# Performance work log

Hardware: AMD Instinct MI355X
Metric: run time of the kernel (lower is better)

Reference implementation:

```python
import jax, jax.numpy as jnp
import numpy as np

N_RAYS = 8192
M = 524288
GX, GY, GZ = 160, 160, 128
NFEAT = 12
POS_PE, VIEW_PE = 10, 4
WIDTH = 128
POS_DIM = 3 + 3 * POS_PE * 2      # 63
VIEW_DIM = 3 + 3 * VIEW_PE * 2    # 27
DIM0 = NFEAT + POS_DIM            # 75
ACT_SHIFT = float(np.log(1.0 / (1.0 - 1e-6) - 1.0))  # density bias shift from alpha_init
INTERVAL = 0.5                    # stepsize * voxel_size_ratio
XYZ_MIN, XYZ_MAX = -1.0, 1.0


def posemb(x, n_pe):
    # x: [N,3] -> [N, 3 + 3*n_pe*2], matching cat([x, sin(x*freq), cos(x*freq)])
    freq = 2.0 ** jnp.arange(n_pe, dtype=x.dtype)
    xf = (x[..., None] * freq).reshape(x.shape[0], -1)
    return jnp.concatenate([x, jnp.sin(xf), jnp.cos(xf)], axis=-1)


def trilinear(grid, xyz):
    # grid: [X,Y,Z,C]; xyz: [M,3] in world coords. align_corners=True bilinear (grid_sample).
    sz_f = jnp.array(grid.shape[:3], jnp.float32)
    sz_i = jnp.array(grid.shape[:3], jnp.int32)
    t = (xyz - XYZ_MIN) / (XYZ_MAX - XYZ_MIN) * (sz_f - 1.0)
    t = jnp.clip(t, 0.0, sz_f - 1.0)
    i0 = jnp.clip(jnp.floor(t).astype(jnp.int32), 0, sz_i - 2)
    f = t - i0.astype(t.dtype)
    out = jnp.zeros((xyz.shape[0], grid.shape[-1]), t.dtype)
    for dx in (0, 1):
        for dy in (0, 1):
            for dz in (0, 1):
                w = ((f[:, 0] if dx else 1.0 - f[:, 0])
                     * (f[:, 1] if dy else 1.0 - f[:, 1])
                     * (f[:, 2] if dz else 1.0 - f[:, 2]))
                out = out + w[:, None] * grid[i0[:, 0] + dx, i0[:, 1] + dy, i0[:, 2] + dz]
    return out


def mask_lookup(mask, xyz):
    # nearest-neighbor maskcache_lookup: ijk = round(xyz*scale + shift)
    sz_f = jnp.array(mask.shape, jnp.float32)
    scale = (sz_f - 1.0) / (XYZ_MAX - XYZ_MIN)
    shift = -XYZ_MIN * scale
    ijk = jnp.clip(jnp.round(xyz * scale + shift).astype(jnp.int32), 0,
                   jnp.array(mask.shape, jnp.int32) - 1)
    return mask[ijk[:, 0], ijk[:, 1], ijk[:, 2]]


def alphas2weights(alpha, ray_id, n_rays):
    # segmented T_i = prod_{j<i in ray}(1-alpha_j); weights = T*alpha (ray_id sorted)
    log1a = jnp.log(jnp.clip(1.0 - alpha, 1e-10, 1.0))
    excl = jnp.cumsum(log1a) - log1a                      # global exclusive cumsum
    seg_tot = jax.ops.segment_sum(log1a, ray_id, num_segments=n_rays)
    seg_start = jnp.cumsum(seg_tot) - seg_tot             # exclusive prefix over rays
    T = jnp.exp(excl - seg_start[ray_id])
    weights = T * alpha
    alphainv_last = jnp.exp(seg_tot)
    return weights, alphainv_last


def setup_inputs() -> dict:
    key = jax.random.key(0)
    ks = jax.random.split(key, 16)
    xyz = jax.random.uniform(ks[0], (M, 3), jnp.float32) * (XYZ_MAX - XYZ_MIN) + XYZ_MIN
    ray_id = jnp.sort(jax.random.randint(ks[1], (M,), 0, N_RAYS))
    viewdirs = jax.random.normal(ks[2], (N_RAYS, 3), jnp.float32)
    viewdirs = viewdirs / jnp.linalg.norm(viewdirs, axis=-1, keepdims=True)
    mask = jax.random.uniform(ks[3], (GX, GY, GZ)) > 0.1
    density = jax.random.normal(ks[4], (GX, GY, GZ), jnp.float32) * 0.5
    k0 = jax.random.normal(ks[5], (GX, GY, GZ, NFEAT), jnp.float32) * 0.1
    s = 0.05
    W0 = jax.random.normal(ks[6], (DIM0, WIDTH), jnp.float32) * s
    b0 = jnp.zeros((WIDTH,), jnp.float32)
    W1 = jax.random.normal(ks[7], (WIDTH, WIDTH), jnp.float32) * s
    b1 = jnp.zeros((WIDTH,), jnp.float32)
    W2 = jax.random.normal(ks[8], (WIDTH, WIDTH), jnp.float32) * s
    b2 = jnp.zeros((WIDTH,), jnp.float32)
    Wr = jax.random.normal(ks[9], (WIDTH + VIEW_DIM, 3), jnp.float32) * s
    br = jnp.zeros((3,), jnp.float32)
    return {"xyz": xyz, "ray_id": ray_id, "viewdirs": viewdirs, "mask": mask,
            "density": density, "k0": k0, "W0": W0, "b0": b0, "W1": W1, "b1": b1,
            "W2": W2, "b2": b2, "Wr": Wr, "br": br}


def reference(xyz, ray_id, viewdirs, mask, density, k0, W0, b0, W1, b1, W2, b2, Wr, br):
    # 1) empty-space skipping via mask cache (kept as multiplicative mask for static shapes)
    m = mask_lookup(mask, xyz).astype(xyz.dtype)
    # 2) trilinear density query + raw2alpha
    d = trilinear(density[..., None], xyz)[:, 0]
    alpha = 1.0 - (1.0 + jnp.exp(d + ACT_SHIFT)) ** (-INTERVAL)
    alpha = alpha * m
    # 3) segmented alpha compositing (Alphas2Weights)
    weights, alphainv_last = alphas2weights(alpha, ray_id, N_RAYS)
    # 4) feature query + view MLP -> rgb
    feat = trilinear(k0, xyz)                              # [M, NFEAT]
    h = jnp.concatenate([feat, posemb(xyz, POS_PE)], -1)   # [M, DIM0]
    h = jax.nn.relu(h @ W0 + b0)
    h = jax.nn.relu(h @ W1 + b1)
    h = jax.nn.relu(h @ W2 + b2)
    ve = posemb(viewdirs, VIEW_PE)[ray_id]                 # [M, VIEW_DIM]
    rgb = jax.nn.sigmoid(jnp.concatenate([h, ve], -1) @ Wr + br)
    # 5) composite per ray + white background
    rgb_marched = jax.ops.segment_sum(weights[:, None] * rgb, ray_id, num_segments=N_RAYS)
    rgb_marched = rgb_marched + alphainv_last[:, None] * 1.0
    return rgb_marched
```

## Files before the change

### kernel.cpp

```cpp
#include <hip/hip_runtime.h>
#include <hip/hip_bf16.h>

#define M_SAMPLES 524288
#define NRAYS 8192
#define GXD 160
#define GYD 160
#define GZD 128
#define GYZ (GYD*GZD)
#define NVOX (GXD*GYD*GZD)
#define ACT_SHIFT -13.81550955796f
#define ROWA 136
#define ROWB 136
#define SAMP 64

typedef __bf16 bf16x8 __attribute__((ext_vector_type(8)));
typedef float f32x4 __attribute__((ext_vector_type(4)));
typedef float f32x16 __attribute__((ext_vector_type(16)));
typedef float f32v2 __attribute__((ext_vector_type(2)));

static __device__ inline unsigned short f2bf(float f){
  __hip_bfloat16 h = __float2bfloat16(f);
  unsigned short u; __builtin_memcpy(&u, &h, 2); return u;
}
static __device__ inline float flo(unsigned int u){ return __uint_as_float(u << 16); }
static __device__ inline float fhi(unsigned int u){ return __uint_as_float(u & 0xffff0000u); }

#if defined(__has_builtin)
#if __has_builtin(__builtin_amdgcn_cvt_pk_bf16_f32)
#define HAVE_PK_BF16 1
#endif
#if __has_builtin(__builtin_amdgcn_cvt_pk_f32_fp8) && __has_builtin(__builtin_amdgcn_cvt_pk_fp8_f32)
#define HAVE_FP8 1
#endif
#endif

static __device__ inline unsigned int packbf(float a, float b){
#ifdef HAVE_PK_BF16
  typedef __bf16 bf16v2 __attribute__((ext_vector_type(2)));
  bf16v2 r = __builtin_amdgcn_cvt_pk_bf16_f32(a, b);
  unsigned int u; __builtin_memcpy(&u, &r, 4); return u;
#else
  return (unsigned int)f2bf(a) | ((unsigned int)f2bf(b) << 16);
#endif
}

struct Tri {
  int ix, iy, iz;
  float wx0, wx1, wy0, wy1, wz0, wz1;
};
static __device__ inline Tri tri_setup(float x, float y, float z){
  Tri t;
  float tx = (x+1.f)*0.5f*(float)(GXD-1); tx = fminf(fmaxf(tx,0.f),(float)(GXD-1));
  float ty = (y+1.f)*0.5f*(float)(GYD-1); ty = fminf(fmaxf(ty,0.f),(float)(GYD-1));
  float tz = (z+1.f)*0.5f*(float)(GZD-1); tz = fminf(fmaxf(tz,0.f),(float)(GZD-1));
  t.ix = min((int)tx, GXD-2); t.iy = min((int)ty, GYD-2); t.iz = min((int)tz, GZD-2);
  float fx = tx-t.ix, fy = ty-t.iy, fz = tz-t.iz;
  t.wx0 = 1.f-fx; t.wx1 = fx; t.wy0 = 1.f-fy; t.wy1 = fy; t.wz0 = 1.f-fz; t.wz1 = fz;
  return t;
}

#define NB_REPACK (NVOX/256)
#define NB_W      184
#define NB_RT     (NRAYS/256)
__global__ __launch_bounds__(256) void k_prep(
    const float* __restrict__ density, const float* __restrict__ k0,
    uint4* __restrict__ packed,
    const unsigned int* __restrict__ mw, int* __restrict__ flag,
    const float* __restrict__ W0, const float* __restrict__ W1,
    const float* __restrict__ W2, const float* __restrict__ Wr,
    const float* __restrict__ br,
    unsigned short* __restrict__ wt0, unsigned short* __restrict__ wt1,
    unsigned short* __restrict__ wt2, unsigned short* __restrict__ wtr,
    const float* __restrict__ vd, float* __restrict__ rayterm3)
{
  int b = blockIdx.x;
  if(b < NB_REPACK){
    int v = b*256 + threadIdx.x;
    const float4* kp = (const float4*)(k0 + (size_t)v*12);
    float4 a = kp[0], bb = kp[1], c = kp[2];
#ifdef HAVE_FP8
    uint4 o;
    o.x = __float_as_uint(density[v]);
    int w;
    w = __builtin_amdgcn_cvt_pk_fp8_f32(a.x, a.y, 0, false);
    w = __builtin_amdgcn_cvt_pk_fp8_f32(a.z, a.w, w, true);
    o.y = (unsigned int)w;
    w = __builtin_amdgcn_cvt_pk_fp8_f32(bb.x, bb.y, 0, false);
    w = __builtin_amdgcn_cvt_pk_fp8_f32(bb.z, bb.w, w, true);
    o.z = (unsigned int)w;
    w = __builtin_amdgcn_cvt_pk_fp8_f32(c.x, c.y, 0, false);
    w = __builtin_amdgcn_cvt_pk_fp8_f32(c.z, c.w, w, true);
    o.w = (unsigned int)w;
    packed[v] = o;
#else
    uint4 o0, o1;
    o0.x = __float_as_uint(density[v]);
    o0.y = packbf(a.x, a.y); o0.z = packbf(a.z, a.w); o0.w = packbf(bb.x, bb.y);
    o1.x = packbf(bb.z, bb.w); o1.y = packbf(c.x, c.y); o1.z = packbf(c.z, c.w);
    o1.w = 0;
    packed[(size_t)v*2]   = o0;
    packed[(size_t)v*2+1] = o1;
#endif
    return;
  }
  if(b == NB_REPACK){
    unsigned int v = mw[threadIdx.x & 63];
    unsigned long long any = __ballot(v > 1u);
    if(threadIdx.x == 0) *flag = (any != 0ull) ? 1 : 0;
    return;
  }
  if(b < NB_REPACK + 1 + NB_W){
    int t = (b - NB_REPACK - 1)*256 + threadIdx.x;
    if(t < 128*96){
      int n = t/96, k = t%96;
      wt0[t] = f2bf((k < 75) ? W0[k*128 + n] : 0.f);
    } else if(t < 128*96 + 16384){
      int j = t - 128*96; int n = j/128, k = j%128;
      wt1[j] = f2bf(W1[k*128 + n]);
    } else if(t < 128*96 + 32768){
      int j = t - 128*96 - 16384; int n = j/128, k = j%128;
      wt2[j] = f2bf(W2[k*128 + n]);
    } else if(t < 128*96 + 32768 + 16*128){
      int j = t - 128*96 - 32768; int n = j/128, k = j%128;
      wtr[j] = f2bf((n < 3) ? Wr[k*3 + n] : 0.f);
    }
    return;
  }
  int ray = (b - NB_REPACK - 1 - NB_W)*256 + threadIdx.x;
  if(ray >= NRAYS) return;
  float v0 = vd[ray*3+0], v1 = vd[ray*3+1], v2 = vd[ray*3+2];
  float vej[27];
  vej[0] = v0; vej[1] = v1; vej[2] = v2;
  #pragma unroll
  for(int ci = 0; ci < 3; ++ci){
    float xv = (ci == 0) ? v0 : ((ci == 1) ? v1 : v2);
    #pragma unroll
    for(int p = 0; p < 4; ++p){
      float arg = xv * (float)(1 << p);
      vej[3 + ci*4 + p]  = __sinf(arg);
      vej[15 + ci*4 + p] = __cosf(arg);
    }
  }
  float rt0 = br[0], rt1 = br[1], rt2 = br[2];
  #pragma unroll
  for(int j = 0; j < 27; ++j){
    const float* wr = Wr + (128 + j)*3;
    rt0 += vej[j]*wr[0]; rt1 += vej[j]*wr[1]; rt2 += vej[j]*wr[2];
  }
  rayterm3[ray*3+0] = rt0; rayterm3[ray*3+1] = rt1; rayterm3[ray*3+2] = rt2;
}

template<int KDIM, int SROW>
static __device__ __forceinline__ void mfma_layer(const unsigned short* src,
    const bf16x8* wf, f32x16& acc0, f32x16& acc1, int ln, int kh)
{
  constexpr int NS = KDIM/16;
  const unsigned short* abase0 = src + (ln)*SROW + kh*8;
  const unsigned short* abase1 = src + (32 + ln)*SROW + kh*8;
  f32x16 z = {0.f,0.f,0.f,0.f,0.f,0.f,0.f,0.f,0.f,0.f,0.f,0.f,0.f,0.f,0.f,0.f};
  acc0 = z; acc1 = z;
  __builtin_amdgcn_s_setprio(1);
  #pragma unroll
  for(int st = 0; st < NS; ++st){
    bf16x8 a0 = *(const bf16x8*)(abase0 + st*16);
    bf16x8 a1 = *(const bf16x8*)(abase1 + st*16);
    acc0 = __builtin_amdgcn_mfma_f32_32x32x16_bf16(wf[st], a0, acc0, 0, 0, 0);
    acc1 = __builtin_amdgcn_mfma_f32_32x32x16_bf16(wf[st], a1, acc1, 0, 0, 0);
  }
  __builtin_amdgcn_s_setprio(0);
}

template<int NS>
static __device__ __forceinline__ void load_wf(const unsigned short* wbase, bf16x8* wf){
  #pragma unroll
  for(int st = 0; st < NS; ++st) wf[st] = *(const bf16x8*)(wbase + st*16);
}

template<int DROW>
static __device__ __forceinline__ void epilogue(const f32x16& acc0, const f32x16& acc1,
    unsigned short* dst, const float* __restrict__ bias, int tile_n, int ln, int kh)
{
  float4 bv[4];
  #pragma unroll
  for(int g = 0; g < 4; ++g) bv[g] = *(const float4*)(bias + tile_n*32 + g*8 + kh*4);
  #pragma unroll
  for(int rep = 0; rep < 2; ++rep){
    const f32x16& acc = rep ? acc1 : acc0;
    int scol = rep*32 + ln;
    #pragma unroll
    for(int g = 0; g < 4; ++g){
      int n0 = tile_n*32 + g*8 + kh*4;
      unsigned int lo = packbf(fmaxf(acc[4*g+0] + bv[g].x, 0.f), fmaxf(acc[4*g+1] + bv[g].y, 0.f));
      unsigned int hi = packbf(fmaxf(acc[4*g+2] + bv[g].z, 0.f), fmaxf(acc[4*g+3] + bv[g].w, 0.f));
      unsigned long long o = (unsigned long long)lo | ((unsigned long long)hi << 32);
      *(unsigned long long*)(dst + scol*DROW + n0) = o;
    }
  }
}

template<int PACKED>
__global__ __launch_bounds__(256, 4) void k_mlp(const float* __restrict__ xyz,
    const uint4* __restrict__ packed,
    const float* __restrict__ density, const float* __restrict__ k0,
    const void* __restrict__ mask, const int* __restrict__ flag,
    const int* __restrict__ ray_id,
    const unsigned short* __restrict__ wt0, const unsigned short* __restrict__ wt1,
    const unsigned short* __restrict__ wt2, const unsigned short* __restrict__ wtr,
    const float* __restrict__ b0, const float* __restrict__ b1,
    const float* __restrict__ b2,
    const float* __restrict__ rayterm3, float4* __restrict__ rgba_out)
{
  __shared__ alignas(16) unsigned short hA[SAMP*ROWA];
  __shared__ alignas(16) unsigned short hB[SAMP*ROWB];
  __shared__ float red[SAMP][4];
  __shared__ int ray_s[SAMP];

  int tid = threadIdx.x;
  int lane = tid & 63, wave = tid >> 6;
  int blk = blockIdx.x*SAMP;
  int ln = lane & 31, kh = lane >> 5;

  bf16x8 wf[8];
  load_wf<6>(wt0 + (wave*32 + ln)*96 + kh*8, wf);

  {
    int smp = tid >> 2, corner = tid & 3;
    int i = blk + smp;
    float x = xyz[3*i+0], y = xyz[3*i+1], z = xyz[3*i+2];
    Tri t = tri_setup(x, y, z);
    int dx = corner & 1, dy = corner >> 1;
    float wxy = (dx ? t.wx1 : t.wx0) * (dy ? t.wy1 : t.wy0);
    float w0 = wxy*t.wz0, w1 = wxy*t.wz1;
    size_t vox = (size_t)((t.ix+dx)*GYZ + (t.iy+dy)*GZD + t.iz);
    float pd;
    float pf[12];
#ifdef HAVE_FP8
    if(PACKED){
      uint4 q0 = packed[vox], q1 = packed[vox+1];
      pd = w0*__uint_as_float(q0.x) + w1*__uint_as_float(q1.x);
      f32v2 a, b;
      a = __builtin_amdgcn_cvt_pk_f32_fp8((int)q0.y, false);
      b = __builtin_amdgcn_cvt_pk_f32_fp8((int)q1.y, false);
      pf[0] = w0*a.x + w1*b.x;  pf[1] = w0*a.y + w1*b.y;
      a = __builtin_amdgcn_cvt_pk_f32_fp8((int)q0.y, true);
      b = __builtin_amdgcn_cvt_pk_f32_fp8((int)q1.y, true);
      pf[2] = w0*a.x + w1*b.x;  pf[3] = w0*a.y + w1*b.y;
      a = __builtin_amdgcn_cvt_pk_f32_fp8((int)q0.z, false);
      b = __builtin_amdgcn_cvt_pk_f32_fp8((int)q1.z, false);
      pf[4] = w0*a.x + w1*b.x;  pf[5] = w0*a.y + w1*b.y;
      a = __builtin_amdgcn_cvt_pk_f32_fp8((int)q0.z, true);
      b = __builtin_amdgcn_cvt_pk_f32_fp8((int)q1.z, true);
      pf[6] = w0*a.x + w1*b.x;  pf[7] = w0*a.y + w1*b.y;
      a = __builtin_amdgcn_cvt_pk_f32_fp8((int)q0.w, false);
      b = __builtin_amdgcn_cvt_pk_f32_fp8((int)q1.w, false);
      pf[8] = w0*a.x + w1*b.x;  pf[9] = w0*a.y + w1*b.y;
      a = __builtin_amdgcn_cvt_pk_f32_fp8((int)q0.w, true);
      b = __builtin_amdgcn_cvt_pk_f32_fp8((int)q1.w, true);
      pf[10]= w0*a.x + w1*b.x;  pf[11]= w0*a.y + w1*b.y;
    }
#else
    if(PACKED){
      const uint4* pv = packed + vox*2;
      uint4 q0 = pv[0], q1 = pv[1], q2 = pv[2], q3 = pv[3];
      pd = w0*__uint_as_float(q0.x) + w1*__uint_as_float(q2.x);
      pf[0]  = w0*flo(q0.y) + w1*flo(q2.y);  pf[1]  = w0*fhi(q0.y) + w1*fhi(q2.y);
      pf[2]  = w0*flo(q0.z) + w1*flo(q2.z);  pf[3]  = w0*fhi(q0.z) + w1*fhi(q2.z);
      pf[4]  = w0*flo(q0.w) + w1*flo(q2.w);  pf[5]  = w0*fhi(q0.w) + w1*fhi(q2.w);
      pf[6]  = w0*flo(q1.x) + w1*flo(q3.x);  pf[7]  = w0*fhi(q1.x) + w1*fhi(q3.x);
      pf[8]  = w0*flo(q1.y) + w1*flo(q3.y);  pf[9]  = w0*fhi(q1.y) + w1*fhi(q3.y);
      pf[10] = w0*flo(q1.z) + w1*flo(q3.z);  pf[11] = w0*fhi(q1.z) + w1*fhi(q3.z);
    }
#endif
    if(!PACKED){
      pd = w0*density[vox] + w1*density[vox+1];
      const float4* v = (const float4*)(k0 + vox*12);
      float4 a0 = v[0], a1 = v[1], a2 = v[2];
      float4 c0 = v[3], c1 = v[4], c2 = v[5];
      pf[0] = w0*a0.x + w1*c0.x;  pf[1] = w0*a0.y + w1*c0.y;
      pf[2] = w0*a0.z + w1*c0.z;  pf[3] = w0*a0.w + w1*c0.w;
      pf[4] = w0*a1.x + w1*c1.x;  pf[5] = w0*a1.y + w1*c1.y;
      pf[6] = w0*a1.z + w1*c1.z;  pf[7] = w0*a1.w + w1*c1.w;
      pf[8] = w0*a2.x + w1*c2.x;  pf[9] = w0*a2.y + w1*c2.y;
      pf[10]= w0*a2.z + w1*c2.z;  pf[11]= w0*a2.w + w1*c2.w;
    }
    #pragma unroll
    for(int m2 = 1; m2 < 4; m2 <<= 1){
      pd += __shfl_xor(pd, m2);
      #pragma unroll
      for(int j = 0; j < 12; ++j) pf[j] += __shfl_xor(pf[j], m2);
    }
    if(corner == 0){
      int mx = (int)rintf(x*79.5f + 79.5f); mx = min(max(mx,0), GXD-1);
      int my = (int)rintf(y*79.5f + 79.5f); my = min(max(my,0), GYD-1);
      int mz = (int)rintf(z*63.5f + 63.5f); mz = min(max(mz,0), GZD-1);
      int midx = mx*GYZ + my*GZD + mz;
      bool mm = (*flag) ? (((const unsigned char*)mask)[midx] != 0)
                        : (((const int*)mask)[midx] != 0);
      float e = __expf(pd + ACT_SHIFT);
      float alpha = 1.f - rsqrtf(1.f + e);
      if(!mm) alpha = 0.f;
      red[smp][3] = alpha;
      unsigned int d[8];
      #pragma unroll
      for(int j = 0; j < 6; ++j) d[j] = packbf(pf[2*j], pf[2*j+1]);
      d[6] = packbf(x, y);
      d[7] = packbf(z, __sinf(x));
      uint4* p = (uint4*)(hA + smp*ROWA);
      p[0] = make_uint4(d[0],d[1],d[2],d[3]);
      p[1] = make_uint4(d[4],d[5],d[6],d[7]);
    } else if(corner == 1){
      uint4* p = (uint4*)(hA + smp*ROWA + 80);
      p[0] = make_uint4(0,0,0,0);
      p[1] = make_uint4(0,0,0,0);
      ray_s[smp] = ray_id[i];
    }
  }

  {
    int smp = tid & 63, chunk = 1 + (tid >> 6);
    int i2 = blk + smp;
    float x = xyz[3*i2+0], y = xyz[3*i2+1], z = xyz[3*i2+2];
    float vv[16];
    #pragma unroll
    for(int j = 0; j < 16; ++j){
      int c = chunk*16 + j;
      float r;
      if(c >= 75) r = 0.f;
      else {
        int q = (c < 45) ? (c-15) : (c-45);
        int ci = q/10, p = q - ci*10;
        float xv = (ci == 0) ? x : ((ci == 1) ? y : z);
        float a = xv * (float)(1 << p);
        r = (c < 45) ? __sinf(a) : __cosf(a);
      }
      vv[j] = r;
    }
    unsigned int d[8];
    #pragma unroll
    for(int j = 0; j < 8; ++j) d[j] = packbf(vv[2*j], vv[2*j+1]);
    uint4* p = (uint4*)(hA + smp*ROWA + chunk*16);
    p[0] = make_uint4(d[0],d[1],d[2],d[3]);
    p[1] = make_uint4(d[4],d[5],d[6],d[7]);
  }
  __syncthreads();

  f32x16 acc0, acc1;

  mfma_layer<96, ROWA>(hA, wf, acc0, acc1, ln, kh);
  load_wf<8>(wt1 + (wave*32 + ln)*128 + kh*8, wf);
  epilogue<ROWB>(acc0, acc1, hB, b0, wave, ln, kh);
  __syncthreads();

  mfma_layer<128, ROWB>(hB, wf, acc0, acc1, ln, kh);
  load_wf<8>(wt2 + (wave*32 + ln)*128 + kh*8, wf);
  epilogue<ROWA>(acc0, acc1, hA, b1, wave, ln, kh);
  __syncthreads();

  int col = lane & 15, q4 = lane >> 4;
  mfma_layer<128, ROWA>(hA, wf, acc0, acc1, ln, kh);
  bf16x8 hw[4];
  {
    const unsigned short* wr = wtr + col*128 + q4*8;
    #pragma unroll
    for(int ks = 0; ks < 4; ++ks) hw[ks] = *(const bf16x8*)(wr + ks*32);
  }
  epilogue<ROWB>(acc0, acc1, hB, b2, wave, ln, kh);
  __syncthreads();

  {
    int mt = wave;
    f32x4 acc = {0.f, 0.f, 0.f, 0.f};
    const unsigned short* arow = hB + (mt*16 + col)*ROWB + q4*8;
    __builtin_amdgcn_s_setprio(1);
    #pragma unroll
    for(int ks = 0; ks < 4; ++ks){
      bf16x8 af = *(const bf16x8*)(arow + ks*32);
      acc = __builtin_amdgcn_mfma_f32_16x16x32_bf16(af, hw[ks], acc, 0, 0, 0);
    }
    __builtin_amdgcn_s_setprio(0);
    if(col < 3){
      #pragma unroll
      for(int r = 0; r < 4; ++r){
        int sl = mt*16 + q4*4 + r;
        float v = acc[r] + rayterm3[ray_s[sl]*3 + col];
        red[sl][col] = __fdividef(1.f, 1.f + __expf(-v));
      }
    }
  }
  __syncthreads();

  if(tid < SAMP){
    rgba_out[blk + tid] = make_float4(red[tid][0], red[tid][1], red[tid][2], red[tid][3]);
  }
}

__global__ __launch_bounds__(256) void k_comp2(const int* __restrict__ ray_id,
    const float4* __restrict__ rgba, float* __restrict__ out)
{
  int r = blockIdx.x*4 + (threadIdx.x >> 6);
  int lane = threadIdx.x & 63;
  int lo = 0, hi = M_SAMPLES;
  while(lo < hi){ int mid = (lo+hi) >> 1; if(ray_id[mid] < r) lo = mid+1; else hi = mid; }
  int s = lo;
  int lo2 = s, hi2 = M_SAMPLES;
  while(lo2 < hi2){ int mid = (lo2+hi2) >> 1; if(ray_id[mid] < r+1) lo2 = mid+1; else hi2 = mid; }
  int e = lo2;

  float carry = 1.f;
  float ar = 0.f, ag = 0.f, ab = 0.f;
  for(int base = s; base < e; base += 64){
    int idx = base + lane;
    float4 c = (idx < e) ? rgba[idx] : make_float4(0.f,0.f,0.f,0.f);
    float a = c.w;
    float incl = 1.f - a;
    #pragma unroll
    for(int d2 = 1; d2 < 64; d2 <<= 1){
      float t = __shfl_up(incl, d2);
      if(lane >= d2) incl *= t;
    }
    float excl = __shfl_up(incl, 1);
    if(lane == 0) excl = 1.f;
    float w = carry * excl * a;
    ar += w*c.x; ag += w*c.y; ab += w*c.z;
    carry *= __shfl(incl, 63);
  }
  #pragma unroll
  for(int m2 = 1; m2 < 64; m2 <<= 1){
    ar += __shfl_xor(ar, m2);
    ag += __shfl_xor(ag, m2);
    ab += __shfl_xor(ab, m2);
  }
  if(lane == 0){
    out[3*r+0] = ar + carry;
    out[3*r+1] = ag + carry;
    out[3*r+2] = ab + carry;
  }
}

extern "C" void kernel_launch(void* const* d_in, const int* in_sizes, int n_in,
                              void* d_out, int out_size, void* d_ws, size_t ws_size,
                              hipStream_t stream)
{
  const float* xyz      = (const float*)d_in[0];
  const int*   ray_id   = (const int*)  d_in[1];
  const float* viewdirs = (const float*)d_in[2];
  const void*  mask     =               d_in[3];
  const float* density  = (const float*)d_in[4];
  const float* k0       = (const float*)d_in[5];
  const float* W0 = (const float*)d_in[6];  const float* b0 = (const float*)d_in[7];
  const float* W1 = (const float*)d_in[8];  const float* b1 = (const float*)d_in[9];
  const float* W2 = (const float*)d_in[10]; const float* b2 = (const float*)d_in[11];
  const float* Wr = (const float*)d_in[12]; const float* br = (const float*)d_in[13];
  float* out = (float*)d_out;

  char* ws = (char*)d_ws;
  size_t off = 0;
  auto take = [&](size_t nbytes) -> void* {
    void* p = ws + off;
    off = (off + nbytes + 255) & ~(size_t)255;
    return p;
  };
  int*            flag     = (int*)           take(4);
  unsigned short* wt0      = (unsigned short*)take(128*96*2);
  unsigned short* wt1      = (unsigned short*)take(128*128*2);
  unsigned short* wt2      = (unsigned short*)take(128*128*2);
  unsigned short* wtr      = (unsigned short*)take(16*128*2);
  float*          rayterm3 = (float*)         take((size_t)NRAYS*3*4);
  float4*         rgba_ws  = (float4*)        take((size_t)M_SAMPLES*16);
#ifdef HAVE_FP8
  uint4*          packed   = (uint4*)         take((size_t)NVOX*16);
#else
  uint4*          packed   = (uint4*)         take((size_t)NVOX*32);
#endif
  bool use_packed = (ws_size >= off);

  k_prep<<<NB_REPACK + 1 + NB_W + NB_RT, 256, 0, stream>>>(
      density, k0, packed, (const unsigned int*)mask, flag,
      W0, W1, W2, Wr, br, wt0, wt1, wt2, wtr, viewdirs, rayterm3);
  if(use_packed){
    k_mlp<1><<<M_SAMPLES/SAMP, 256, 0, stream>>>(xyz, packed, density, k0, mask, flag,
                                                 ray_id, wt0, wt1, wt2, wtr,
                                                 b0, b1, b2, rayterm3, rgba_ws);
  } else {
    k_mlp<0><<<M_SAMPLES/SAMP, 256, 0, stream>>>(xyz, packed, density, k0, mask, flag,
                                                 ray_id, wt0, wt1, wt2, wtr,
                                                 b0, b1, b2, rayterm3, rgba_ws);
  }
  k_comp2<<<NRAYS/4, 256, 0, stream>>>(ray_id, rgba_ws, out);
}
```

Baseline: 417.1 us.

## Make MLP kernel persistent with register-resident weights and prefetched next-tile gathers

Converts k_mlp into a persistent kernel with 768 blocks that loop over the 64-sample tiles. Layer-1 and layer-2 weight fragments stay in registers across tiles, and biases are staged once in shared memory. Each iteration issues the next tile's xyz loads, grid gathers, mask lookup and ray_id load before running the current tile's MFMA layers, so gather latency overlaps compute. In exchange it uses many more registers, lowers occupancy to 3 blocks per SIMD group, and adds an extra barrier per tile.

```diff
diff --git a/kernel.cpp b/kernel.cpp
--- a/kernel.cpp
+++ b/kernel.cpp
@@ -12,6 +12,8 @@
 #define ROWA 136
 #define ROWB 136
 #define SAMP 64
+#define NTILES (M_SAMPLES/SAMP)
+#define GRID_MLP 768
 
 typedef __bf16 bf16x8 __attribute__((ext_vector_type(8)));
 typedef float f32x4 __attribute__((ext_vector_type(4)));
@@ -152,7 +154,7 @@
 
 template<int KDIM, int SROW>
 static __device__ __forceinline__ void mfma_layer(const unsigned short* src,
-    const bf16x8* wf, f32x16& acc0, f32x16& acc1, int ln, int kh)
+    const f32x4* wf, f32x16& acc0, f32x16& acc1, int ln, int kh)
 {
   constexpr int NS = KDIM/16;
   const unsigned short* abase0 = src + (ln)*SROW + kh*8;
@@ -164,25 +166,20 @@
   for(int st = 0; st < NS; ++st){
     bf16x8 a0 = *(const bf16x8*)(abase0 + st*16);
     bf16x8 a1 = *(const bf16x8*)(abase1 + st*16);
-    acc0 = __builtin_amdgcn_mfma_f32_32x32x16_bf16(wf[st], a0, acc0, 0, 0, 0);
-    acc1 = __builtin_amdgcn_mfma_f32_32x32x16_bf16(wf[st], a1, acc1, 0, 0, 0);
+    bf16x8 wv = __builtin_bit_cast(bf16x8, wf[st]);
+    acc0 = __builtin_amdgcn_mfma_f32_32x32x16_bf16(wv, a0, acc0, 0, 0, 0);
+    acc1 = __builtin_amdgcn_mfma_f32_32x32x16_bf16(wv, a1, acc1, 0, 0, 0);
   }
   __builtin_amdgcn_s_setprio(0);
-}
-
-template<int NS>
-static __device__ __forceinline__ void load_wf(const unsigned short* wbase, bf16x8* wf){
-  #pragma unroll
-  for(int st = 0; st < NS; ++st) wf[st] = *(const bf16x8*)(wbase + st*16);
 }
 
 template<int DROW>
 static __device__ __forceinline__ void epilogue(const f32x16& acc0, const f32x16& acc1,
-    unsigned short* dst, const float* __restrict__ bias, int tile_n, int ln, int kh)
+    unsigned short* dst, const float* sbias, int tile_n, int ln, int kh)
 {
   float4 bv[4];
   #pragma unroll
-  for(int g = 0; g < 4; ++g) bv[g] = *(const float4*)(bias + tile_n*32 + g*8 + kh*4);
+  for(int g = 0; g < 4; ++g) bv[g] = *(const float4*)(sbias + tile_n*32 + g*8 + kh*4);
   #pragma unroll
   for(int rep = 0; rep < 2; ++rep){
     const f32x16& acc = rep ? acc1 : acc0;
@@ -199,7 +196,7 @@
 }
 
 template<int PACKED>
-__global__ __launch_bounds__(256, 4) void k_mlp(const float* __restrict__ xyz,
+__global__ __launch_bounds__(256, 3) void k_mlp(const float* __restrict__ xyz,
     const uint4* __restrict__ packed,
     const float* __restrict__ density, const float* __restrict__ k0,
     const void* __restrict__ mask, const int* __restrict__ flag,
@@ -214,183 +211,257 @@
   __shared__ alignas(16) unsigned short hB[SAMP*ROWB];
   __shared__ float red[SAMP][4];
   __shared__ int ray_s[SAMP];
+  __shared__ alignas(16) float sb[384];
 
   int tid = threadIdx.x;
   int lane = tid & 63, wave = tid >> 6;
-  int blk = blockIdx.x*SAMP;
   int ln = lane & 31, kh = lane >> 5;
-
-  bf16x8 wf[8];
-  load_wf<6>(wt0 + (wave*32 + ln)*96 + kh*8, wf);
-
+  int col = lane & 15, q4 = lane >> 4;
+  int smp_a = tid >> 2, corner = tid & 3;
+  int dxc = corner & 1, dyc = corner >> 1;
+  int smp_b = tid & 63, chunk = 1 + (tid >> 6);
+  int flg = *flag;
+
+  if(tid < 96){
+    int which = tid >> 5, j = tid & 31;
+    const float* bs = (which == 0) ? b0 : ((which == 1) ? b1 : b2);
+    *(float4*)(sb + which*128 + j*4) = *(const float4*)(bs + j*4);
+  }
+
+  f32x4 wf1[8], wf2[8];
   {
-    int smp = tid >> 2, corner = tid & 3;
-    int i = blk + smp;
-    float x = xyz[3*i+0], y = xyz[3*i+1], z = xyz[3*i+2];
-    Tri t = tri_setup(x, y, z);
-    int dx = corner & 1, dy = corner >> 1;
-    float wxy = (dx ? t.wx1 : t.wx0) * (dy ? t.wy1 : t.wy0);
-    float w0 = wxy*t.wz0, w1 = wxy*t.wz1;
-    size_t vox = (size_t)((t.ix+dx)*GYZ + (t.iy+dy)*GZD + t.iz);
-    float pd;
-    float pf[12];
+    const unsigned short* w1b = wt1 + (wave*32 + ln)*128 + kh*8;
+    const unsigned short* w2b = wt2 + (wave*32 + ln)*128 + kh*8;
+    #pragma unroll
+    for(int st = 0; st < 8; ++st){
+      wf1[st] = *(const f32x4*)(w1b + st*16);
+      wf2[st] = *(const f32x4*)(w2b + st*16);
+    }
+  }
+  #pragma unroll
+  for(int st = 0; st < 8; ++st){
+    asm volatile("" : "+v"(wf1[st]));
+    asm volatile("" : "+v"(wf2[st]));
+  }
+
+  float ax, ay, az, bx, by, bz;
+  float cw0 = 0.f, cw1 = 0.f;
+  size_t voxs = 0;
+  uint4 q0 = {}, q1 = {};
+#ifndef HAVE_FP8
+  uint4 q2 = {}, q3 = {};
+#endif
+  int rid = 0; unsigned int mv = 0;
+
+  auto prefetch_gather = [&](int TT){
+    Tri tr = tri_setup(ax, ay, az);
+    float wxy = (dxc ? tr.wx1 : tr.wx0) * (dyc ? tr.wy1 : tr.wy0);
+    cw0 = wxy*tr.wz0; cw1 = wxy*tr.wz1;
+    voxs = (size_t)((tr.ix+dxc)*GYZ + (tr.iy+dyc)*GZD + tr.iz);
+    if(PACKED){
 #ifdef HAVE_FP8
-    if(PACKED){
-      uint4 q0 = packed[vox], q1 = packed[vox+1];
-      pd = w0*__uint_as_float(q0.x) + w1*__uint_as_float(q1.x);
-      f32v2 a, b;
-      a = __builtin_amdgcn_cvt_pk_f32_fp8((int)q0.y, false);
-      b = __builtin_amdgcn_cvt_pk_f32_fp8((int)q1.y, false);
-      pf[0] = w0*a.x + w1*b.x;  pf[1] = w0*a.y + w1*b.y;
-      a = __builtin_amdgcn_cvt_pk_f32_fp8((int)q0.y, true);
-      b = __builtin_amdgcn_cvt_pk_f32_fp8((int)q1.y, true);
-      pf[2] = w0*a.x + w1*b.x;  pf[3] = w0*a.y + w1*b.y;
-      a = __builtin_amdgcn_cvt_pk_f32_fp8((int)q0.z, false);
-      b = __builtin_amdgcn_cvt_pk_f32_fp8((int)q1.z, false);
-      pf[4] = w0*a.x + w1*b.x;  pf[5] = w0*a.y + w1*b.y;
-      a = __builtin_amdgcn_cvt_pk_f32_fp8((int)q0.z, true);
-      b = __builtin_amdgcn_cvt_pk_f32_fp8((int)q1.z, true);
-      pf[6] = w0*a.x + w1*b.x;  pf[7] = w0*a.y + w1*b.y;
-      a = __builtin_amdgcn_cvt_pk_f32_fp8((int)q0.w, false);
-      b = __builtin_amdgcn_cvt_pk_f32_fp8((int)q1.w, false);
-      pf[8] = w0*a.x + w1*b.x;  pf[9] = w0*a.y + w1*b.y;
-      a = __builtin_amdgcn_cvt_pk_f32_fp8((int)q0.w, true);
-      b = __builtin_amdgcn_cvt_pk_f32_fp8((int)q1.w, true);
-      pf[10]= w0*a.x + w1*b.x;  pf[11]= w0*a.y + w1*b.y;
-    }
+      q0 = packed[voxs]; q1 = packed[voxs+1];
 #else
-    if(PACKED){
-      const uint4* pv = packed + vox*2;
-      uint4 q0 = pv[0], q1 = pv[1], q2 = pv[2], q3 = pv[3];
-      pd = w0*__uint_as_float(q0.x) + w1*__uint_as_float(q2.x);
-      pf[0]  = w0*flo(q0.y) + w1*flo(q2.y);  pf[1]  = w0*fhi(q0.y) + w1*fhi(q2.y);
-      pf[2]  = w0*flo(q0.z) + w1*flo(q2.z);  pf[3]  = w0*fhi(q0.z) + w1*fhi(q2.z);
-      pf[4]  = w0*flo(q0.w) + w1*flo(q2.w);  pf[5]  = w0*fhi(q0.w) + w1*fhi(q2.w);
-      pf[6]  = w0*flo(q1.x) + w1*flo(q3.x);  pf[7]  = w0*fhi(q1.x) + w1*fhi(q3.x);
-      pf[8]  = w0*flo(q1.y) + w1*flo(q3.y);  pf[9]  = w0*fhi(q1.y) + w1*fhi(q3.y);
-      pf[10] = w0*flo(q1.z) + w1*flo(q3.z);  pf[11] = w0*fhi(q1.z) + w1*fhi(q3.z);
-    }
-#endif
-    if(!PACKED){
-      pd = w0*density[vox] + w1*density[vox+1];
-      const float4* v = (const float4*)(k0 + vox*12);
-      float4 a0 = v[0], a1 = v[1], a2 = v[2];
-      float4 c0 = v[3], c1 = v[4], c2 = v[5];
-      pf[0] = w0*a0.x + w1*c0.x;  pf[1] = w0*a0.y + w1*c0.y;
-      pf[2] = w0*a0.z + w1*c0.z;  pf[3] = w0*a0.w + w1*c0.w;
-      pf[4] = w0*a1.x + w1*c1.x;  pf[5] = w0*a1.y + w1*c1.y;
-      pf[6] = w0*a1.z + w1*c1.z;  pf[7] = w0*a1.w + w1*c1.w;
-      pf[8] = w0*a2.x + w1*c2.x;  pf[9] = w0*a2.y + w1*c2.y;
-      pf[10]= w0*a2.z + w1*c2.z;  pf[11]= w0*a2.w + w1*c2.w;
-    }
-    #pragma unroll
-    for(int m2 = 1; m2 < 4; m2 <<= 1){
-      pd += __shfl_xor(pd, m2);
-      #pragma unroll
-      for(int j = 0; j < 12; ++j) pf[j] += __shfl_xor(pf[j], m2);
+      const uint4* pv = packed + voxs*2;
+      q0 = pv[0]; q1 = pv[1]; q2 = pv[2]; q3 = pv[3];
+#endif
     }
     if(corner == 0){
-      int mx = (int)rintf(x*79.5f + 79.5f); mx = min(max(mx,0), GXD-1);
-      int my = (int)rintf(y*79.5f + 79.5f); my = min(max(my,0), GYD-1);
-      int mz = (int)rintf(z*63.5f + 63.5f); mz = min(max(mz,0), GZD-1);
+      int mx = (int)rintf(ax*79.5f + 79.5f); mx = min(max(mx,0), GXD-1);
+      int my = (int)rintf(ay*79.5f + 79.5f); my = min(max(my,0), GYD-1);
+      int mz = (int)rintf(az*63.5f + 63.5f); mz = min(max(mz,0), GZD-1);
       int midx = mx*GYZ + my*GZD + mz;
-      bool mm = (*flag) ? (((const unsigned char*)mask)[midx] != 0)
-                        : (((const int*)mask)[midx] != 0);
-      float e = __expf(pd + ACT_SHIFT);
-      float alpha = 1.f - rsqrtf(1.f + e);
-      if(!mm) alpha = 0.f;
-      red[smp][3] = alpha;
+      mv = flg ? (unsigned int)(((const unsigned char*)mask)[midx])
+               : ((const unsigned int*)mask)[midx];
+    } else if(corner == 1){
+      rid = ray_id[TT*SAMP + smp_a];
+    }
+  };
+
+  int t = blockIdx.x;
+  {
+    int ia = t*SAMP + smp_a;
+    ax = xyz[3*ia+0]; ay = xyz[3*ia+1]; az = xyz[3*ia+2];
+    int ib = t*SAMP + smp_b;
+    bx = xyz[3*ib+0]; by = xyz[3*ib+1]; bz = xyz[3*ib+2];
+  }
+  prefetch_gather(t);
+
+  for(; t < NTILES; t += GRID_MLP){
+    int nt = t + GRID_MLP;
+    bool has_next = nt < NTILES;
+    int blk = t*SAMP;
+
+    float nax=0.f, nay=0.f, naz=0.f, nbx=0.f, nby=0.f, nbz=0.f;
+    if(has_next){
+      int ia = nt*SAMP + smp_a;
+      nax = xyz[3*ia+0]; nay = xyz[3*ia+1]; naz = xyz[3*ia+2];
+      int ib = nt*SAMP + smp_b;
+      nbx = xyz[3*ib+0]; nby = xyz[3*ib+1]; nbz = xyz[3*ib+2];
+    }
+    __builtin_amdgcn_sched_barrier(0);
+
+    {
+      float pd;
+      float pf[12];
+#ifdef HAVE_FP8
+      if(PACKED){
+        pd = cw0*__uint_as_float(q0.x) + cw1*__uint_as_float(q1.x);
+        f32v2 a, b;
+        a = __builtin_amdgcn_cvt_pk_f32_fp8((int)q0.y, false);
+        b = __builtin_amdgcn_cvt_pk_f32_fp8((int)q1.y, false);
+        pf[0] = cw0*a.x + cw1*b.x;  pf[1] = cw0*a.y + cw1*b.y;
+        a = __builtin_amdgcn_cvt_pk_f32_fp8((int)q0.y, true);
+        b = __builtin_amdgcn_cvt_pk_f32_fp8((int)q1.y, true);
+        pf[2] = cw0*a.x + cw1*b.x;  pf[3] = cw0*a.y + cw1*b.y;
+        a = __builtin_amdgcn_cvt_pk_f32_fp8((int)q0.z, false);
+        b = __builtin_amdgcn_cvt_pk_f32_fp8((int)q1.z, false);
+        pf[4] = cw0*a.x + cw1*b.x;  pf[5] = cw0*a.y + cw1*b.y;
+        a = __builtin_amdgcn_cvt_pk_f32_fp8((int)q0.z, true);
+        b = __builtin_amdgcn_cvt_pk_f32_fp8((int)q1.z, true);
+        pf[6] = cw0*a.x + cw1*b.x;  pf[7] = cw0*a.y + cw1*b.y;
+        a = __builtin_amdgcn_cvt_pk_f32_fp8((int)q0.w, false);
+        b = __builtin_amdgcn_cvt_pk_f32_fp8((int)q1.w, false);
+        pf[8] = cw0*a.x + cw1*b.x;  pf[9] = cw0*a.y + cw1*b.y;
+        a = __builtin_amdgcn_cvt_pk_f32_fp8((int)q0.w, true);
+        b = __builtin_amdgcn_cvt_pk_f32_fp8((int)q1.w, true);
+        pf[10]= cw0*a.x + cw1*b.x;  pf[11]= cw0*a.y + cw1*b.y;
+      }
+#else
+      if(PACKED){
+        pd = cw0*__uint_as_float(q0.x) + cw1*__uint_as_float(q2.x);
+        pf[0]  = cw0*flo(q0.y) + cw1*flo(q2.y);  pf[1]  = cw0*fhi(q0.y) + cw1*fhi(q2.y);
+        pf[2]  = cw0*flo(q0.z) + cw1*flo(q2.z);  pf[3]  = cw0*fhi(q0.z) + cw1*fhi(q2.z);
+        pf[4]  = cw0*flo(q0.w) + cw1*flo(q2.w);  pf[5]  = cw0*fhi(q0.w) + cw1*fhi(q2.w);
+        pf[6]  = cw0*flo(q1.x) + cw1*flo(q3.x);  pf[7]  = cw0*fhi(q1.x) + cw1*fhi(q3.x);
+        pf[8]  = cw0*flo(q1.y) + cw1*flo(q3.y);  pf[9]  = cw0*fhi(q1.y) + cw1*fhi(q3.y);
+        pf[10] = cw0*flo(q1.z) + cw1*flo(q3.z);  pf[11] = cw0*fhi(q1.z) + cw1*fhi(q3.z);
+      }
+#endif
+      if(!PACKED){
+        pd = cw0*density[voxs] + cw1*density[voxs+1];
+        const float4* v = (const float4*)(k0 + voxs*12);
+        float4 a0 = v[0], a1 = v[1], a2 = v[2];
+        float4 c0 = v[3], c1 = v[4], c2 = v[5];
+        pf[0] = cw0*a0.x + cw1*c0.x;  pf[1] = cw0*a0.y + cw1*c0.y;
+        pf[2] = cw0*a0.z + cw1*c0.z;  pf[3] = cw0*a0.w + cw1*c0.w;
+        pf[4] = cw0*a1.x + cw1*c1.x;  pf[5] = cw0*a1.y + cw1*c1.y;
+        pf[6] = cw0*a1.z + cw1*c1.z;  pf[7] = cw0*a1.w + cw1*c1.w;
+        pf[8] = cw0*a2.x + cw1*c2.x;  pf[9] = cw0*a2.y + cw1*c2.y;
+        pf[10]= cw0*a2.z + cw1*c2.z;  pf[11]= cw0*a2.w + cw1*c2.w;
+      }
+      #pragma unroll
+      for(int m2 = 1; m2 < 4; m2 <<= 1){
+        pd += __shfl_xor(pd, m2);
+        #pragma unroll
+        for(int j = 0; j < 12; ++j) pf[j] += __shfl_xor(pf[j], m2);
+      }
+      if(corner == 0){
+        bool mm = (mv != 0u);
+        float e = __expf(pd + ACT_SHIFT);
+        float alpha = 1.f - rsqrtf(1.f + e);
+        if(!mm) alpha = 0.f;
+        red[smp_a][3] = alpha;
+        unsigned int d[8];
+        #pragma unroll
+        for(int j = 0; j < 6; ++j) d[j] = packbf(pf[2*j], pf[2*j+1]);
+        d[6] = packbf(ax, ay);
+        d[7] = packbf(az, __sinf(ax));
+        uint4* p = (uint4*)(hA + smp_a*ROWA);
+        p[0] = make_uint4(d[0],d[1],d[2],d[3]);
+        p[1] = make_uint4(d[4],d[5],d[6],d[7]);
+      } else if(corner == 1){
+        uint4* p = (uint4*)(hA + smp_a*ROWA + 80);
+        p[0] = make_uint4(0,0,0,0);
+        p[1] = make_uint4(0,0,0,0);
+        ray_s[smp_a] = rid;
+      }
+    }
+
+    {
+      float vv[16];
+      #pragma unroll
+      for(int j = 0; j < 16; ++j){
+        int c = chunk*16 + j;
+        float r;
+        if(c >= 75) r = 0.f;
+        else {
+          int q = (c < 45) ? (c-15) : (c-45);
+          int ci = q/10, p = q - ci*10;
+          float xv = (ci == 0) ? bx : ((ci == 1) ? by : bz);
+          float a = xv * (float)(1 << p);
+          r = (c < 45) ? __sinf(a) : __cosf(a);
+        }
+        vv[j] = r;
+      }
       unsigned int d[8];
       #pragma unroll
-      for(int j = 0; j < 6; ++j) d[j] = packbf(pf[2*j], pf[2*j+1]);
-      d[6] = packbf(x, y);
-      d[7] = packbf(z, __sinf(x));
-      uint4* p = (uint4*)(hA + smp*ROWA);
+      for(int j = 0; j < 8; ++j) d[j] = packbf(vv[2*j], vv[2*j+1]);
+      uint4* p = (uint4*)(hA + smp_b*ROWA + chunk*16);
       p[0] = make_uint4(d[0],d[1],d[2],d[3]);
       p[1] = make_uint4(d[4],d[5],d[6],d[7]);
-    } else if(corner == 1){
-      uint4* p = (uint4*)(hA + smp*ROWA + 80);
-      p[0] = make_uint4(0,0,0,0);
-      p[1] = make_uint4(0,0,0,0);
-      ray_s[smp] = ray_id[i];
-    }
-  }
-
-  {
-    int smp = tid & 63, chunk = 1 + (tid >> 6);
-    int i2 = blk + smp;
-    float x = xyz[3*i2+0], y = xyz[3*i2+1], z = xyz[3*i2+2];
-    float vv[16];
-    #pragma unroll
-    for(int j = 0; j < 16; ++j){
-      int c = chunk*16 + j;
-      float r;
-      if(c >= 75) r = 0.f;
-      else {
-        int q = (c < 45) ? (c-15) : (c-45);
-        int ci = q/10, p = q - ci*10;
-        float xv = (ci == 0) ? x : ((ci == 1) ? y : z);
-        float a = xv * (float)(1 << p);
-        r = (c < 45) ? __sinf(a) : __cosf(a);
-      }
-      vv[j] = r;
-    }
-    unsigned int d[8];
-    #pragma unroll
-    for(int j = 0; j < 8; ++j) d[j] = packbf(vv[2*j], vv[2*j+1]);
-    uint4* p = (uint4*)(hA + smp*ROWA + chunk*16);
-    p[0] = make_uint4(d[0],d[1],d[2],d[3]);
-    p[1] = make_uint4(d[4],d[5],d[6],d[7]);
-  }
-  __syncthreads();
-
-  f32x16 acc0, acc1;
-
-  mfma_layer<96, ROWA>(hA, wf, acc0, acc1, ln, kh);
-  load_wf<8>(wt1 + (wave*32 + ln)*128 + kh*8, wf);
-  epilogue<ROWB>(acc0, acc1, hB, b0, wave, ln, kh);
-  __syncthreads();
-
-  mfma_layer<128, ROWB>(hB, wf, acc0, acc1, ln, kh);
-  load_wf<8>(wt2 + (wave*32 + ln)*128 + kh*8, wf);
-  epilogue<ROWA>(acc0, acc1, hA, b1, wave, ln, kh);
-  __syncthreads();
-
-  int col = lane & 15, q4 = lane >> 4;
-  mfma_layer<128, ROWA>(hA, wf, acc0, acc1, ln, kh);
-  bf16x8 hw[4];
-  {
-    const unsigned short* wr = wtr + col*128 + q4*8;
-    #pragma unroll
-    for(int ks = 0; ks < 4; ++ks) hw[ks] = *(const bf16x8*)(wr + ks*32);
-  }
-  epilogue<ROWB>(acc0, acc1, hB, b2, wave, ln, kh);
-  __syncthreads();
-
-  {
-    int mt = wave;
-    f32x4 acc = {0.f, 0.f, 0.f, 0.f};
-    const unsigned short* arow = hB + (mt*16 + col)*ROWB + q4*8;
-    __builtin_amdgcn_s_setprio(1);
-    #pragma unroll
-    for(int ks = 0; ks < 4; ++ks){
-      bf16x8 af = *(const bf16x8*)(arow + ks*32);
-      acc = __builtin_amdgcn_mfma_f32_16x16x32_bf16(af, hw[ks], acc, 0, 0, 0);
-    }
-    __builtin_amdgcn_s_setprio(0);
+    }
+    __syncthreads();
+
+    f32x4 wf0[6], hwf[4];
+    {
+      const unsigned short* w0b = wt0 + (wave*32 + ln)*96 + kh*8;
+      #pragma unroll
+      for(int st = 0; st < 6; ++st) wf0[st] = *(const f32x4*)(w0b + st*16);
+      const unsigned short* wrb = wtr + col*128 + q4*8;
+      #pragma unroll
+      for(int ks = 0; ks < 4; ++ks) hwf[ks] = *(const f32x4*)(wrb + ks*32);
+    }
+    float rt[4] = {0.f, 0.f, 0.f, 0.f};
     if(col < 3){
       #pragma unroll
-      for(int r = 0; r < 4; ++r){
-        int sl = mt*16 + q4*4 + r;
-        float v = acc[r] + rayterm3[ray_s[sl]*3 + col];
-        red[sl][col] = __fdividef(1.f, 1.f + __expf(-v));
-      }
-    }
-  }
-  __syncthreads();
-
-  if(tid < SAMP){
-    rgba_out[blk + tid] = make_float4(red[tid][0], red[tid][1], red[tid][2], red[tid][3]);
+      for(int r = 0; r < 4; ++r)
+        rt[r] = rayterm3[ray_s[wave*16 + q4*4 + r]*3 + col];
+    }
+    __builtin_amdgcn_sched_barrier(0);
+
+    if(has_next){
+      ax = nax; ay = nay; az = naz; bx = nbx; by = nby; bz = nbz;
+      prefetch_gather(nt);
+    }
+    __builtin_amdgcn_sched_barrier(0);
+
+    f32x16 acc0, acc1;
+    mfma_layer< 96, ROWA>(hA, wf0, acc0, acc1, ln, kh);
+    epilogue<ROWB>(acc0, acc1, hB, sb,       wave, ln, kh);
+    __syncthreads();
+    mfma_layer<128, ROWB>(hB, wf1, acc0, acc1, ln, kh);
+    epilogue<ROWA>(acc0, acc1, hA, sb + 128, wave, ln, kh);
+    __syncthreads();
+    mfma_layer<128, ROWA>(hA, wf2, acc0, acc1, ln, kh);
+    epilogue<ROWB>(acc0, acc1, hB, sb + 256, wave, ln, kh);
+    __syncthreads();
+
+    {
+      f32x4 acc = {0.f, 0.f, 0.f, 0.f};
+      const unsigned short* arow = hB + (wave*16 + col)*ROWB + q4*8;
+      __builtin_amdgcn_s_setprio(1);
+      #pragma unroll
+      for(int ks = 0; ks < 4; ++ks){
+        bf16x8 af = *(const bf16x8*)(arow + ks*32);
+        acc = __builtin_amdgcn_mfma_f32_16x16x32_bf16(af, __builtin_bit_cast(bf16x8, hwf[ks]), acc, 0, 0, 0);
+      }
+      __builtin_amdgcn_s_setprio(0);
+      if(col < 3){
+        #pragma unroll
+        for(int r = 0; r < 4; ++r){
+          int sl = wave*16 + q4*4 + r;
+          float v = acc[r] + rt[r];
+          red[sl][col] = __fdividef(1.f, 1.f + __expf(-v));
+        }
+      }
+    }
+    __syncthreads();
+
+    if(tid < SAMP){
+      rgba_out[blk + tid] = make_float4(red[tid][0], red[tid][1], red[tid][2], red[tid][3]);
+    }
+    __syncthreads();
   }
 }
 
@@ -478,13 +549,13 @@
       density, k0, packed, (const unsigned int*)mask, flag,
       W0, W1, W2, Wr, br, wt0, wt1, wt2, wtr, viewdirs, rayterm3);
   if(use_packed){
-    k_mlp<1><<<M_SAMPLES/SAMP, 256, 0, stream>>>(xyz, packed, density, k0, mask, flag,
-                                                 ray_id, wt0, wt1, wt2, wtr,
-                                                 b0, b1, b2, rayterm3, rgba_ws);
+    k_mlp<1><<<GRID_MLP, 256, 0, stream>>>(xyz, packed, density, k0, mask, flag,
+                                           ray_id, wt0, wt1, wt2, wtr,
+                                           b0, b1, b2, rayterm3, rgba_ws);
   } else {
-    k_mlp<0><<<M_SAMPLES/SAMP, 256, 0, stream>>>(xyz, packed, density, k0, mask, flag,
-                                                 ray_id, wt0, wt1, wt2, wtr,
-                                                 b0, b1, b2, rayterm3, rgba_ws);
+    k_mlp<0><<<GRID_MLP, 256, 0, stream>>>(xyz, packed, density, k0, mask, flag,
+                                           ray_id, wt0, wt1, wt2, wtr,
+                                           b0, b1, b2, rayterm3, rgba_ws);
   }
   k_comp2<<<NRAYS/4, 256, 0, stream>>>(ray_id, rgba_ws, out);
 }
```

Result: slower. 486.3 us (+16.6%).
